# Kernel optimization log

Hardware: AMD Instinct MI355X
Metric: run time of the kernel (lower is better)

The kernel has to match this reference:

```python
import jax, jax.numpy as jnp
import numpy as np

B = 16384      # batch
CNUM = 2048    # codebook entries
K = 8          # topk
D = 10         # emb_dim
M = 50         # meta_dim
UID = 1000000
IID = 1000000
TAU = 10.0


def setup_inputs() -> dict:
    key = jax.random.key(0)
    ks = jax.random.split(key, 14)
    uid_col = jax.random.randint(ks[0], (B, 1), 0, UID, dtype=jnp.int64)
    iid_col = jax.random.randint(ks[1], (B, 1), 0, IID + 1, dtype=jnp.int64)
    x = jnp.concatenate([uid_col, iid_col], axis=1)
    return {
        "x": x,
        "gumbel_u_src": jax.random.uniform(ks[2], (B, CNUM), dtype=jnp.float32),
        "gumbel_u_tgt": jax.random.uniform(ks[3], (B, CNUM), dtype=jnp.float32),
        "src_uid_table": jax.random.normal(ks[4], (UID, D), dtype=jnp.float32),
        "tgt_uid_table": jax.random.normal(ks[5], (UID, D), dtype=jnp.float32),
        "tgt_iid_table": jax.random.normal(ks[6], (IID + 1, D), dtype=jnp.float32),
        "C": jax.random.normal(ks[7], (CNUM, M), dtype=jnp.float32) * 0.01,
        "w1": jax.random.normal(ks[8], (D, M), dtype=jnp.float32) * 0.01,
        "w2": jax.random.normal(ks[9], (M, D), dtype=jnp.float32) * 0.01,
        "mw1": jax.random.normal(ks[10], (D + M, 50), dtype=jnp.float32) * 0.1,
        "mb1": jnp.zeros((50,), dtype=jnp.float32),
        "mw2": jax.random.normal(ks[11], (50, D * D), dtype=jnp.float32) * 0.1,
        "mb2": jnp.zeros((D * D,), dtype=jnp.float32),
    }


def _gumbel_route(u_emb, C, w1, u_noise):
    # u_emb: [B, D] -> logits s_u: [B, CNUM]
    s = jnp.einsum('bm,cm->bc', u_emb @ w1, C)
    g = -jnp.log(-jnp.log(u_noise + 1e-20) + 1e-20)  # gumbel noise
    gw = jax.nn.softmax((s + g) / TAU, axis=-1)       # F.gumbel_softmax, hard=False
    tw, ti = jax.lax.top_k(gw, K)                     # [B, K]
    c_u = C[ti]                                       # [B, K, M] codebook gather
    return tw, ti, c_u


def reference(x, gumbel_u_src, gumbel_u_tgt, src_uid_table, tgt_uid_table,
              tgt_iid_table, C, w1, w2, mw1, mb1, mw2, mb2):
    # ---- stage == 'test_meta' ----
    # target-side interest embedding ('test_interst' path)
    tuid = tgt_uid_table[x[:, 0]]                      # [B, D]
    tw_t, _, c_t = _gumbel_route(tuid, C, w1, gumbel_u_tgt)
    tuid_ins = ((c_t * tw_t[..., None]).sum(axis=1)) @ w2   # [B, D]
    # source-side routing ('test_meta' path of InterstEmbedding)
    uid = src_uid_table[x[:, 0]]                       # [B, D]
    tw_s, _, c_s = _gumbel_route(uid, C, w1, gumbel_u_src)
    src_fea = jnp.broadcast_to(uid[:, None, :], (uid.shape[0], K, D))  # [B, K, D]
    inp = jnp.concatenate([c_s, src_fea], axis=-1)     # [B, K, M+D] = [B, K, 60]
    h = jax.nn.relu(inp @ mw1 + mb1)                   # [B, K, 50]
    mapping = (h @ mw2 + mb2).reshape(-1, K, D, D)     # per-sample hypernet weights
    src_emb = jnp.einsum('bkd,bkde->bke', src_fea, mapping)  # [B, K, D]
    pre_emb = (src_emb * tw_s[..., None]).sum(axis=1)  # [B, D]
    fin_emb = tuid_ins + pre_emb                       # [B, D]
    iid_emb = tgt_iid_table[x[:, 1]]                   # [B, D]
    return jnp.sum(fin_emb * iid_emb, axis=-1)         # [B]
```

## Files before the change

### kernel.cpp

```cpp
#include <hip/hip_runtime.h>
#include <hip/hip_bf16.h>


#define BROWS 16384
#define CNUM  2048
#define KSEL  8
#define DIMD  10
#define MDIM  50
#define TAUI  0.1f

typedef float    f32x4 __attribute__((ext_vector_type(4)));
typedef _Float16 half8 __attribute__((ext_vector_type(8)));
typedef float    flt2  __attribute__((ext_vector_type(2)));
typedef unsigned int u32;
typedef unsigned long long u64;

__device__ __forceinline__ u32 pkrtz(float a, float b) {
    auto h = __builtin_amdgcn_cvt_pkrtz(a, b);
    union { decltype(h) v; u32 u; } c; c.v = h; return c.u;
}
__device__ __forceinline__ float gnoise(float u) {
    return -__logf(-__logf(u + 1e-20f) + 1e-20f);
}

__global__ void cvtC(const float* __restrict__ Cm, u32* __restrict__ C16) {
    const int j = blockIdx.x * 256 + threadIdx.x;
    const int w = j & 3, l = (j >> 2) & 63, pl = (j >> 8) & 1, Tg = j >> 9;
    const int cand = Tg * 16 + (l & 15);
    const int kk = pl * 16 + ((l >> 4) << 2) + w;
    const int k = 2 * kk;
    const float a = (k < MDIM)     ? Cm[cand*MDIM + k]     : 0.f;
    const float b = (k + 1 < MDIM) ? Cm[cand*MDIM + k + 1] : 0.f;
    C16[j] = pkrtz(a, b);
}

__global__ __launch_bounds__(256, 8)
void mf_route(const int* __restrict__ x32,
              const float* __restrict__ gsrc,
              const float* __restrict__ gtgt,
              const float* __restrict__ suid,
              const float* __restrict__ tuid,
              const float* __restrict__ Cm,
              const float* __restrict__ w1,
              const u32* __restrict__ C16,
              float* __restrict__ gTW,
              int*   __restrict__ gTI)
{
    __shared__ __align__(16) float smem[2432];
    __shared__ int sFlag;
    float* sPf  = smem;
    u32*   T48u = (u32*)(smem + 832);
    float* T48l = smem + 1600;
    float* TS   = smem + 2368;

    const int tid  = threadIdx.x;
    const int row0 = blockIdx.x * 8;

    if (tid == 0) sFlag = 1;
    __syncthreads();
    if (tid < 128) { if (x32[2*tid+1] != 0) atomicAnd(&sFlag, 0); }
    __syncthreads();
    const int is64 = sFlag;

    for (int t = tid; t < 16*52; t += 256) {
        const int rt = t / 52, mm = t - rt*52;
        float v = 0.f;
        if (mm < MDIM) {
            const int r = row0 + (rt >> 1);
            const int uidx = is64 ? x32[4*r] : x32[2*r];
            const float* tab = (rt & 1) ? suid : tuid;
            #pragma unroll
            for (int d = 0; d < DIMD; ++d) v += tab[uidx*DIMD + d] * w1[d*MDIM + mm];
        }
        sPf[t] = v;
    }
    __syncthreads();

    const int lane = tid & 63, wv = tid >> 6;
    const int lr = lane & 15, lk = lane >> 4;
    const int rt = lr;
    const float* up = ((lr & 1) ? gsrc : gtgt) + (size_t)(row0 + (lr >> 1)) * CNUM;

    half8 b0, b1;
    {
        union { u32 u[4]; half8 v; } c0, c1;
        #pragma unroll
        for (int jj = 0; jj < 4; ++jj) {
            const int k0 = lk*8 + jj*2;
            c0.u[jj] = pkrtz(sPf[rt*52 + k0], sPf[rt*52 + k0 + 1]);
            const int k1 = 32 + lk*8 + jj*2;
            const float e0 = (k1     < 52) ? sPf[rt*52 + k1]     : 0.f;
            const float e1 = (k1 + 1 < 52) ? sPf[rt*52 + k1 + 1] : 0.f;
            c1.u[jj] = pkrtz(e0, e1);
        }
        b0 = c0.v; b1 = c1.v;
    }

    float ts = 0.f;
    float q0=-3.4e38f,q1=-3.4e38f,q2=-3.4e38f,q3=-3.4e38f,
          q4=-3.4e38f,q5=-3.4e38f,q6=-3.4e38f,q7=-3.4e38f;

    for (int t = 0; t < 32; ++t) {
        const int cb = wv*512 + t*16;
        const f32x4 u4 = *(const f32x4*)(up + cb + lk*4);
        const u32* cp = C16 + (size_t)((wv*32 + t)*128 + lane)*4;
        const half8 a0 = *(const half8*)cp;
        const half8 a1 = *(const half8*)(cp + 256);
        f32x4 acc = {0.f, 0.f, 0.f, 0.f};
        acc = __builtin_amdgcn_mfma_f32_16x16x32_f16(a0, b0, acc, 0, 0, 0);
        acc = __builtin_amdgcn_mfma_f32_16x16x32_f16(a1, b1, acc, 0, 0, 0);
        const int cg = cb + lk*4;
        #pragma unroll
        for (int r4 = 0; r4 < 4; ++r4) {
            const float l = (acc[r4] + gnoise(u4[r4])) * TAUI;
            ts += __expf(l);
            const float xs = __uint_as_float(
                (__float_as_uint(l) & 0xFFFFF800u) | (u32)(cg + r4));
            q0 = fmaxf(q0, fminf(q1, xs));
            q1 = fmaxf(q1, fminf(q2, xs));
            q2 = fmaxf(q2, fminf(q3, xs));
            q3 = fmaxf(q3, fminf(q4, xs));
            q4 = fmaxf(q4, fminf(q5, xs));
            q5 = fmaxf(q5, fminf(q6, xs));
            q6 = fmaxf(q6, fminf(q7, xs));
            q7 = fmaxf(q7, xs);
        }
    }

    {
        float tss = ts;
        tss += __shfl_xor(tss, 16); tss += __shfl_xor(tss, 32);
        if (lk == 0) TS[rt*4 + wv] = tss;
        #pragma unroll
        for (int k = 0; k < 12; ++k) {
            float gm = fmaxf(q7, __shfl_xor(q7, 16));
            gm = fmaxf(gm, __shfl_xor(gm, 32));
            if (q7 == gm) {
                T48u[rt*48 + wv*12 + k] = __float_as_uint(q7);
                q7=q6; q6=q5; q5=q4; q4=q3; q3=q2; q2=q1; q1=q0; q0=-3.4e38f;
            }
        }
    }
    __syncthreads();

    for (int e = tid; e < 16*48; e += 256) {
        const int ert = e / 48;
        const int idx = (int)(T48u[e] & 2047u);
        const float* pf = sPf + ert*52;
        const float* cr = Cm + idx*MDIM;
        float s = 0.f;
        #pragma unroll
        for (int k2 = 0; k2 < 25; ++k2) {
            flt2 c = *(const flt2*)(cr + k2*2);
            s += pf[2*k2] * c.x + pf[2*k2+1] * c.y;
        }
        const int r = row0 + (ert >> 1);
        const float u = ((ert & 1) ? gsrc : gtgt)[(size_t)r*CNUM + idx];
        T48l[e] = (s + gnoise(u)) * TAUI;
    }
    __syncthreads();

    if (tid < 16) {
        const int r8 = tid;
        const float inv = 1.0f / (TS[r8*4] + TS[r8*4+1] + TS[r8*4+2] + TS[r8*4+3]);
        u64 used = 0;
        for (int k = 0; k < KSEL; ++k) {
            float bl = -3.4e38f; int bi = 1 << 30; int bj = 0;
            for (int j = 0; j < 48; ++j) {
                if ((used >> j) & 1ull) continue;
                const float lv = T48l[r8*48 + j];
                const int   iv = (int)(T48u[r8*48 + j] & 2047u);
                if (lv > bl || (lv == bl && iv < bi)) { bl = lv; bi = iv; bj = j; }
            }
            used |= 1ull << bj;
            const int grt = blockIdx.x*16 + r8;
            gTW[grt*KSEL + k] = __expf(bl) * inv;
            gTI[grt*KSEL + k] = bi;
        }
    }
}

__global__ __launch_bounds__(256, 4)
void mf_epilog(const int* __restrict__ x32,
               const float* __restrict__ suid,
               const float* __restrict__ tiid,
               const float* __restrict__ Cm,
               const float* __restrict__ w2,
               const float* __restrict__ mw1,
               const float* __restrict__ mb1,
               const float* __restrict__ mw2,
               const float* __restrict__ mb2,
               const float* __restrict__ gTW,
               const int*   __restrict__ gTI,
               float* __restrict__ out)
{
    __shared__ int sFlag;
    const int tid = threadIdx.x;
    const int g = tid >> 4, lg = tid & 15;
    const int row = blockIdx.x * 16 + g;

    if (tid == 0) sFlag = 1;
    __syncthreads();
    if (tid < 128) { if (x32[2*tid+1] != 0) atomicAnd(&sFlag, 0); }
    __syncthreads();
    const int is64 = sFlag;

    const int uidx = is64 ? x32[4*row]     : x32[2*row];
    const int iidx = is64 ? x32[4*row + 2] : x32[2*row + 1];

    float uid[10], ti[10];
    #pragma unroll
    for (int d = 0; d < DIMD; ++d) uid[d] = suid[(size_t)uidx*DIMD + d];
    #pragma unroll
    for (int e = 0; e < DIMD; ++e) ti[e] = tiid[(size_t)iidx*DIMD + e];

    float twt[8], tws[8]; int it[8], is_[8];
    #pragma unroll
    for (int k = 0; k < KSEL; ++k) {
        twt[k] = gTW[(row*2)*KSEL + k];     it[k]  = gTI[(row*2)*KSEL + k];
        tws[k] = gTW[(row*2+1)*KSEL + k];   is_[k] = gTI[(row*2+1)*KSEL + k];
    }

    const int j0 = 4*lg;
    const int nj = (j0 + 4 <= MDIM) ? 4 : (j0 < MDIM ? MDIM - j0 : 0);

    float po = 0.f;
    float qt[4] = {0,0,0,0}, w2t[4] = {0,0,0,0}, hb[4] = {0,0,0,0};

    if (nj) {
        {
            flt2 m0 = *(const flt2*)(mb1 + j0);
            hb[0] = m0.x; hb[1] = m0.y;
            if (nj == 4) { flt2 m1 = *(const flt2*)(mb1 + j0 + 2); hb[2] = m1.x; hb[3] = m1.y; }
            #pragma unroll
            for (int d = 0; d < DIMD; ++d) {
                const float* r = mw1 + (MDIM + d)*MDIM + j0;
                flt2 a = *(const flt2*)r;
                hb[0] += uid[d]*a.x; hb[1] += uid[d]*a.y;
                if (nj == 4) { flt2 b = *(const flt2*)(r + 2); hb[2] += uid[d]*b.x; hb[3] += uid[d]*b.y; }
            }
        }
        for (int jj = 0; jj < nj; ++jj) {
            const float* r = w2 + (j0 + jj)*DIMD;
            float s = 0.f;
            #pragma unroll
            for (int p = 0; p < 5; ++p) { flt2 a = *(const flt2*)(r + 2*p); s += a.x*ti[2*p] + a.y*ti[2*p+1]; }
            w2t[jj] = s;
        }
        for (int jj = 0; jj < nj; ++jj) {
            const float* r = mw2 + (size_t)(j0 + jj)*(DIMD*DIMD);
            float s = 0.f;
            #pragma unroll
            for (int d = 0; d < DIMD; ++d) {
                float sd = 0.f;
                #pragma unroll
                for (int p = 0; p < 5; ++p) { flt2 a = *(const flt2*)(r + d*DIMD + 2*p); sd += a.x*ti[2*p] + a.y*ti[2*p+1]; }
                s += uid[d]*sd;
            }
            qt[jj] = s;
        }
        {
            float ws[4] = {0,0,0,0};
            #pragma unroll
            for (int k = 0; k < KSEL; ++k) {
                const float* cr = Cm + (size_t)it[k]*MDIM + j0;
                flt2 a = *(const flt2*)cr;
                ws[0] += twt[k]*a.x; ws[1] += twt[k]*a.y;
                if (nj == 4) { flt2 b = *(const flt2*)(cr + 2); ws[2] += twt[k]*b.x; ws[3] += twt[k]*b.y; }
            }
            for (int jj = 0; jj < nj; ++jj) po += ws[jj]*w2t[jj];
        }
        float hk[8][4];
        #pragma unroll
        for (int k = 0; k < KSEL; ++k)
            #pragma unroll
            for (int jj = 0; jj < 4; ++jj) hk[k][jj] = hb[jj];
        for (int t2 = 0; t2 < MDIM; t2 += 2) {
            const float* r0 = mw1 + t2*MDIM + j0;
            const float* r1 = mw1 + (t2+1)*MDIM + j0;
            flt2 wa0 = *(const flt2*)r0, wb0 = *(const flt2*)(r0 + 2);
            flt2 wa1 = *(const flt2*)r1, wb1 = *(const flt2*)(r1 + 2);
            #pragma unroll
            for (int k = 0; k < KSEL; ++k) {
                flt2 c = *(const flt2*)(Cm + (size_t)is_[k]*MDIM + t2);
                hk[k][0] += c.x*wa0.x + c.y*wa1.x;
                hk[k][1] += c.x*wa0.y + c.y*wa1.y;
                hk[k][2] += c.x*wb0.x + c.y*wb1.x;
                hk[k][3] += c.x*wb0.y + c.y*wb1.y;
            }
        }
        #pragma unroll
        for (int k = 0; k < KSEL; ++k) {
            float s = 0.f;
            for (int jj = 0; jj < nj; ++jj) s += fmaxf(hk[k][jj], 0.f)*qt[jj];
            po += tws[k]*s;
        }
    }
    if (lg == 0) {
        float stw = 0.f;
        #pragma unroll
        for (int k = 0; k < KSEL; ++k) stw += tws[k];
        float bt = 0.f;
        #pragma unroll
        for (int d = 0; d < DIMD; ++d) {
            float sd = 0.f;
            #pragma unroll
            for (int e = 0; e < DIMD; ++e) sd += mb2[d*DIMD + e]*ti[e];
            bt += uid[d]*sd;
        }
        po += stw*bt;
    }
    po += __shfl_xor(po, 1, 16);
    po += __shfl_xor(po, 2, 16);
    po += __shfl_xor(po, 4, 16);
    po += __shfl_xor(po, 8, 16);
    if (lg == 0) out[row] = po;
}

__global__ __launch_bounds__(256, 4)
void mf_fused_fb(const int* __restrict__ x32,
                 const float* __restrict__ gsrc,
                 const float* __restrict__ gtgt,
                 const float* __restrict__ suid,
                 const float* __restrict__ tuid,
                 const float* __restrict__ tiid,
                 const float* __restrict__ Cm,
                 const float* __restrict__ w1,
                 const float* __restrict__ w2,
                 const float* __restrict__ mw1,
                 const float* __restrict__ mb1,
                 const float* __restrict__ mw2,
                 const float* __restrict__ mb2,
                 float* __restrict__ out)
{
    __shared__ __align__(16) float smem[9536];
    __shared__ int sFlag;
    float* sPf  = smem;
    u32*   T24u = (u32*)(smem + 1664);
    float* T24l = smem + 2432;

    const int tid  = threadIdx.x;
    const int row0 = blockIdx.x * 16;

    if (tid == 0) sFlag = 1;
    __syncthreads();
    if (tid < 128) { if (x32[2*tid+1] != 0) atomicAnd(&sFlag, 0); }
    __syncthreads();
    const int is64 = sFlag;

    for (int t = tid; t < 32*52; t += 256) {
        const int rt = t / 52, mm = t - rt*52;
        float v = 0.f;
        if (mm < MDIM) {
            const int r = row0 + (rt >> 1);
            const int uidx = is64 ? x32[4*r] : x32[2*r];
            const float* tab = (rt & 1) ? suid : tuid;
            #pragma unroll
            for (int d = 0; d < DIMD; ++d) v += tab[uidx*DIMD + d] * w1[d*MDIM + mm];
        }
        sPf[t] = v;
    }
    __syncthreads();

    const int lane = tid & 63, wv = tid >> 6;
    const int lr = lane & 15, lk = lane >> 4;
    const int g = wv & 1, h = wv >> 1;
    const int rt = g*16 + lr;
    const float* up = ((lr & 1) ? gsrc : gtgt) + (size_t)(row0 + g*8 + (lr >> 1)) * CNUM;

    half8 b0, b1;
    {
        union { u32 u[4]; half8 v; } c0, c1;
        #pragma unroll
        for (int jj = 0; jj < 4; ++jj) {
            const int k0 = lk*8 + jj*2;
            c0.u[jj] = pkrtz(sPf[rt*52 + k0], sPf[rt*52 + k0 + 1]);
            const int k1 = 32 + lk*8 + jj*2;
            const float e0 = (k1     < 52) ? sPf[rt*52 + k1]     : 0.f;
            const float e1 = (k1 + 1 < 52) ? sPf[rt*52 + k1 + 1] : 0.f;
            c1.u[jj] = pkrtz(e0, e1);
        }
        b0 = c0.v; b1 = c1.v;
    }

    float ts = 0.f;
    float q0=-3.4e38f,q1=-3.4e38f,q2=-3.4e38f,q3=-3.4e38f,
          q4=-3.4e38f,q5=-3.4e38f,q6=-3.4e38f,q7=-3.4e38f;

    for (int t = 0; t < 64; ++t) {
        const int cb = ((t >> 2) << 7) + h*64 + ((t & 3) << 4);
        const float* cr = Cm + (size_t)(cb + lr)*MDIM;
        union { u32 u[4]; half8 v; } c0, c1;
        #pragma unroll
        for (int jj = 0; jj < 4; ++jj) {
            const int k0 = lk*8 + jj*2;
            c0.u[jj] = pkrtz(cr[k0], cr[k0+1]);
            const int k1 = 32 + lk*8 + jj*2;
            const float e0 = (k1     < MDIM) ? cr[k1]   : 0.f;
            const float e1 = (k1 + 1 < MDIM) ? cr[k1+1] : 0.f;
            c1.u[jj] = pkrtz(e0, e1);
        }
        f32x4 acc = {0.f, 0.f, 0.f, 0.f};
        acc = __builtin_amdgcn_mfma_f32_16x16x32_f16(c0.v, b0, acc, 0, 0, 0);
        acc = __builtin_amdgcn_mfma_f32_16x16x32_f16(c1.v, b1, acc, 0, 0, 0);
        const f32x4 u4 = *(const f32x4*)(up + cb + lk*4);
        const int cg = cb + lk*4;
        #pragma unroll
        for (int r4 = 0; r4 < 4; ++r4) {
            const float l = (acc[r4] + gnoise(u4[r4])) * TAUI;
            ts += __expf(l);
            const float xs = __uint_as_float(
                (__float_as_uint(l) & 0xFFFFF800u) | (u32)(cg + r4));
            q0 = fmaxf(q0, fminf(q1, xs));
            q1 = fmaxf(q1, fminf(q2, xs));
            q2 = fmaxf(q2, fminf(q3, xs));
            q3 = fmaxf(q3, fminf(q4, xs));
            q4 = fmaxf(q4, fminf(q5, xs));
            q5 = fmaxf(q5, fminf(q6, xs));
            q6 = fmaxf(q6, fminf(q7, xs));
            q7 = fmaxf(q7, xs);
        }
    }

    {
        float tss = ts;
        tss += __shfl_xor(tss, 16); tss += __shfl_xor(tss, 32);
        if (lk == 0) smem[3200 + rt*2 + h] = tss;
        #pragma unroll
        for (int k = 0; k < 12; ++k) {
            float gm = fmaxf(q7, __shfl_xor(q7, 16));
            gm = fmaxf(gm, __shfl_xor(gm, 32));
            if (q7 == gm) {
                T24u[rt*24 + h*12 + k] = __float_as_uint(q7);
                q7=q6; q6=q5; q5=q4; q4=q3; q3=q2; q2=q1; q1=q0; q0=-3.4e38f;
            }
        }
    }
    __syncthreads();

    for (int e = tid; e < 32*24; e += 256) {
        const int ert = e / 24;
        const int idx = (int)(T24u[e] & 2047u);
        const float* pf = sPf + ert*52;
        const float* cr = Cm + idx*MDIM;
        float s = 0.f;
        #pragma unroll
        for (int k2 = 0; k2 < 25; ++k2) {
            flt2 c = *(const flt2*)(cr + k2*2);
            s += pf[2*k2] * c.x + pf[2*k2+1] * c.y;
        }
        const int r = row0 + (ert >> 1);
        const float u = ((ert & 1) ? gsrc : gtgt)[(size_t)r*CNUM + idx];
        T24l[e] = (s + gnoise(u)) * TAUI;
    }
    __syncthreads();

    if (tid < 32) {
        const int rrt = tid;
        const float inv = 1.0f / (smem[3200 + rrt*2] + smem[3200 + rrt*2 + 1]);
        u32 used = 0;
        for (int k = 0; k < KSEL; ++k) {
            float bl = -3.4e38f; int bi = 1 << 30; int bj = 0;
            for (int j = 0; j < 24; ++j) {
                if ((used >> j) & 1) continue;
                const float lv = T24l[rrt*24 + j];
                const int   iv = (int)(T24u[rrt*24 + j] & 2047u);
                if (lv > bl || (lv == bl && iv < bi)) { bl = lv; bi = iv; bj = j; }
            }
            used |= 1u << bj;
            smem[8832 + rrt*KSEL + k] = __expf(bl) * inv;
            ((int*)smem)[9088 + rrt*KSEL + k] = bi;
        }
    }
    __syncthreads();

    float* sH    = smem;
    float* sQ    = smem + 832;
    float* sUd   = smem + 9344;
    float* sTopW = smem + 8832;
    int*   sTopI = (int*)smem + 9088;

    const int gg = tid >> 4, lg = tid & 15;
    const int row = row0 + gg;
    const int rt_t = gg*2, rt_s = gg*2 + 1;
    const int uidx = is64 ? x32[4*row]     : x32[2*row];
    const int iidx = is64 ? x32[4*row + 2] : x32[2*row + 1];

    if (lg < DIMD) sUd[gg*12 + lg] = suid[uidx*DIMD + lg];
    __syncthreads();

    for (int t = lg; t < MDIM*DIMD; t += 16) {
        const int j = t / DIMD, e = t - j*DIMD;
        float q = 0.f;
        #pragma unroll
        for (int d = 0; d < DIMD; ++d) q += sUd[gg*12 + d] * mw2[j*(DIMD*DIMD) + d*DIMD + e];
        sQ[gg*500 + t] = q;
    }
    for (int mm = lg; mm < MDIM; mm += 16) {
        float v = 0.f;
        #pragma unroll
        for (int k = 0; k < KSEL; ++k)
            v += sTopW[rt_t*KSEL + k] * Cm[sTopI[rt_t*KSEL + k]*MDIM + mm];
        sH[gg*52 + mm] = v;
    }
    __syncthreads();

    float acc_e = 0.f, be = 0.f;
    if (lg < DIMD) {
        for (int m2 = 0; m2 < MDIM; ++m2) acc_e += sH[gg*52 + m2] * w2[m2*DIMD + lg];
        #pragma unroll
        for (int d = 0; d < DIMD; ++d) be += sUd[gg*12 + d] * mb2[d*DIMD + lg];
    }
    __syncthreads();

    for (int k = 0; k < KSEL; ++k) {
        const int   ik = sTopI[rt_s*KSEL + k];
        const float tw = sTopW[rt_s*KSEL + k];
        for (int j = lg; j < MDIM; j += 16) {
            float hh = mb1[j];
            const float* crow = Cm + ik*MDIM;
            for (int t2 = 0; t2 < MDIM; ++t2) hh += crow[t2] * mw1[t2*MDIM + j];
            #pragma unroll
            for (int d = 0; d < DIMD; ++d) hh += sUd[gg*12 + d] * mw1[(MDIM + d)*MDIM + j];
            sH[gg*52 + j] = fmaxf(hh, 0.f);
        }
        __syncthreads();
        if (lg < DIMD) {
            float se = be;
            for (int j = 0; j < MDIM; ++j) se += sH[gg*52 + j] * sQ[gg*500 + j*DIMD + lg];
            acc_e += tw * se;
        }
        __syncthreads();
    }

    float o = 0.f;
    if (lg < DIMD) o = acc_e * tiid[iidx*DIMD + lg];
    #pragma unroll
    for (int k = 8; k >= 1; k >>= 1) o += __shfl_xor(o, k, 16);
    if (lg == 0) out[row] = o;
}

extern "C" void kernel_launch(void* const* d_in, const int* in_sizes, int n_in,
                              void* d_out, int out_size, void* d_ws, size_t ws_size,
                              hipStream_t stream) {
    (void)in_sizes; (void)n_in; (void)out_size;
    const int*   x32  = (const int*)d_in[0];
    const float* gsrc = (const float*)d_in[1];
    const float* gtgt = (const float*)d_in[2];
    const float* suid = (const float*)d_in[3];
    const float* tuid = (const float*)d_in[4];
    const float* tiid = (const float*)d_in[5];
    const float* Cm   = (const float*)d_in[6];
    const float* w1   = (const float*)d_in[7];
    const float* w2   = (const float*)d_in[8];
    const float* mw1  = (const float*)d_in[9];
    const float* mb1  = (const float*)d_in[10];
    const float* mw2  = (const float*)d_in[11];
    const float* mb2  = (const float*)d_in[12];

    if (ws_size >= 655360u * 4u) {
        u32*   C16 = (u32*)d_ws;
        float* gTW = (float*)d_ws + 131072;
        int*   gTI = (int*)d_ws + 393216;
        hipLaunchKernelGGL(cvtC, dim3(512), dim3(256), 0, stream, Cm, C16);
        hipLaunchKernelGGL(mf_route, dim3(BROWS/8), dim3(256), 0, stream,
                           x32, gsrc, gtgt, suid, tuid, Cm, w1, C16, gTW, gTI);
        hipLaunchKernelGGL(mf_epilog, dim3(BROWS/16), dim3(256), 0, stream,
                           x32, suid, tiid, Cm, w2, mw1, mb1, mw2, mb2, gTW, gTI,
                           (float*)d_out);
    } else {
        hipLaunchKernelGGL(mf_fused_fb, dim3(BROWS/16), dim3(256), 0, stream,
                           x32, gsrc, gtgt, suid, tuid, tiid, Cm, w1, w2, mw1, mb1, mw2, mb2,
                           (float*)d_out);
    }
}
```

Before: 283.5 us.

## Stage gumbel noise tiles through LDS with double-buffered async global_load_lds

The per-lane strided global loads of the uniform noise are replaced by coalesced 16-byte global_load_lds transfers into a double-buffered, XOR-swizzled LDS tile. Each step prefetches the next 128-column chunk while the current one feeds the MFMA and top-k work. Column ownership is re-split so every wave covers 32 columns of each 128-column chunk instead of a contiguous 512-column range. This adds 16 KB of LDS per block and a block barrier each iteration, which may lower occupancy and add synchronisation stalls.

```diff
diff --git a/kernel.cpp b/kernel.cpp
--- a/kernel.cpp
+++ b/kernel.cpp
@@ -8,6 +8,7 @@
 #define DIMD  10
 #define MDIM  50
 #define TAUI  0.1f
+#define UOFF  832
 
 typedef float    f32x4 __attribute__((ext_vector_type(4)));
 typedef _Float16 half8 __attribute__((ext_vector_type(8)));
@@ -21,6 +22,12 @@
 }
 __device__ __forceinline__ float gnoise(float u) {
     return -__logf(-__logf(u + 1e-20f) + 1e-20f);
+}
+__device__ __forceinline__ void gload16(const float* g, float* l) {
+    __builtin_amdgcn_global_load_lds(
+        (const __attribute__((address_space(1))) u32*)g,
+        (__attribute__((address_space(3))) u32*)l,
+        16, 0, 0);
 }
 
 __global__ void cvtC(const float* __restrict__ Cm, u32* __restrict__ C16) {
@@ -46,7 +53,7 @@
               float* __restrict__ gTW,
               int*   __restrict__ gTI)
 {
-    __shared__ __align__(16) float smem[2432];
+    __shared__ __align__(16) float smem[UOFF + 4096];
     __shared__ int sFlag;
     float* sPf  = smem;
     u32*   T48u = (u32*)(smem + 832);
@@ -76,10 +83,9 @@
     }
     __syncthreads();
 
-    const int lane = tid & 63, wv = tid >> 6;
+    const int lane = tid & 63, w = tid >> 6;
     const int lr = lane & 15, lk = lane >> 4;
     const int rt = lr;
-    const float* up = ((lr & 1) ? gsrc : gtgt) + (size_t)(row0 + (lr >> 1)) * CNUM;
 
     half8 b0, b1;
     {
@@ -96,47 +102,80 @@
         b0 = c0.v; b1 = c1.v;
     }
 
+    const int jrow = lane >> 5, jc4 = lane & 31;
+    const int rtS0 = 4*w + jrow;
+    const int rtS1 = 4*w + 2 + jrow;
+    const float* usrc0 = ((rtS0 & 1) ? gsrc : gtgt)
+        + (size_t)(row0 + (rtS0 >> 1))*CNUM + ((jc4 ^ (rtS0 & 7)) << 2);
+    const float* usrc1 = ((rtS1 & 1) ? gsrc : gtgt)
+        + (size_t)(row0 + (rtS1 >> 1))*CNUM + ((jc4 ^ (rtS1 & 7)) << 2);
+    float* const udst0a = smem + UOFF +        (4*w    )*128;
+    float* const udst1a = smem + UOFF +        (4*w + 2)*128;
+    float* const udst0b = smem + UOFF + 2048 + (4*w    )*128;
+    float* const udst1b = smem + UOFF + 2048 + (4*w + 2)*128;
+
     float ts = 0.f;
     float q0=-3.4e38f,q1=-3.4e38f,q2=-3.4e38f,q3=-3.4e38f,
           q4=-3.4e38f,q5=-3.4e38f,q6=-3.4e38f,q7=-3.4e38f;
 
-    for (int t = 0; t < 32; ++t) {
-        const int cb = wv*512 + t*16;
-        const f32x4 u4 = *(const f32x4*)(up + cb + lk*4);
-        const u32* cp = C16 + (size_t)((wv*32 + t)*128 + lane)*4;
-        const half8 a0 = *(const half8*)cp;
-        const half8 a1 = *(const half8*)(cp + 256);
-        f32x4 acc = {0.f, 0.f, 0.f, 0.f};
-        acc = __builtin_amdgcn_mfma_f32_16x16x32_f16(a0, b0, acc, 0, 0, 0);
-        acc = __builtin_amdgcn_mfma_f32_16x16x32_f16(a1, b1, acc, 0, 0, 0);
-        const int cg = cb + lk*4;
-        #pragma unroll
-        for (int r4 = 0; r4 < 4; ++r4) {
-            const float l = (acc[r4] + gnoise(u4[r4])) * TAUI;
-            ts += __expf(l);
-            const float xs = __uint_as_float(
-                (__float_as_uint(l) & 0xFFFFF800u) | (u32)(cg + r4));
-            q0 = fmaxf(q0, fminf(q1, xs));
-            q1 = fmaxf(q1, fminf(q2, xs));
-            q2 = fmaxf(q2, fminf(q3, xs));
-            q3 = fmaxf(q3, fminf(q4, xs));
-            q4 = fmaxf(q4, fminf(q5, xs));
-            q5 = fmaxf(q5, fminf(q6, xs));
-            q6 = fmaxf(q6, fminf(q7, xs));
-            q7 = fmaxf(q7, xs);
-        }
+    const int physa = ((w*8)     + lk) ^ (lr & 7);
+    const int physb = ((w*8 + 4) + lk) ^ (lr & 7);
+    const int rbase = UOFF + lr*128;
+
+    gload16(usrc0, udst0a);
+    gload16(usrc1, udst1a);
+    __syncthreads();
+
+    for (int t = 0; t < 16; ++t) {
+        const int bufw = (t & 1) * 2048;
+        const f32x4 u4a = *(const f32x4*)&smem[rbase + bufw + physa*4];
+        const f32x4 u4b = *(const f32x4*)&smem[rbase + bufw + physb*4];
+        if (t + 1 < 16) {
+            const int nb = ((t + 1) & 1) * 2048;
+            gload16(usrc0 + (t + 1)*128, (nb ? udst0b : udst0a));
+            gload16(usrc1 + (t + 1)*128, (nb ? udst1b : udst1a));
+        }
+        #pragma unroll
+        for (int nt = 0; nt < 2; ++nt) {
+            const int cl = w*32 + nt*16;
+            const int Tg = t*8 + w*2 + nt;
+            const u32* cp = C16 + (size_t)(Tg*128 + lane)*4;
+            const half8 a0 = *(const half8*)cp;
+            const half8 a1 = *(const half8*)(cp + 256);
+            f32x4 acc = {0.f, 0.f, 0.f, 0.f};
+            acc = __builtin_amdgcn_mfma_f32_16x16x32_f16(a0, b0, acc, 0, 0, 0);
+            acc = __builtin_amdgcn_mfma_f32_16x16x32_f16(a1, b1, acc, 0, 0, 0);
+            const f32x4 u4 = nt ? u4b : u4a;
+            const int cg = t*128 + cl + lk*4;
+            #pragma unroll
+            for (int r4 = 0; r4 < 4; ++r4) {
+                const float l = (acc[r4] + gnoise(u4[r4])) * TAUI;
+                ts += __expf(l);
+                const float xs = __uint_as_float(
+                    (__float_as_uint(l) & 0xFFFFF800u) | (u32)(cg + r4));
+                q0 = fmaxf(q0, fminf(q1, xs));
+                q1 = fmaxf(q1, fminf(q2, xs));
+                q2 = fmaxf(q2, fminf(q3, xs));
+                q3 = fmaxf(q3, fminf(q4, xs));
+                q4 = fmaxf(q4, fminf(q5, xs));
+                q5 = fmaxf(q5, fminf(q6, xs));
+                q6 = fmaxf(q6, fminf(q7, xs));
+                q7 = fmaxf(q7, xs);
+            }
+        }
+        __syncthreads();
     }
 
     {
         float tss = ts;
         tss += __shfl_xor(tss, 16); tss += __shfl_xor(tss, 32);
-        if (lk == 0) TS[rt*4 + wv] = tss;
+        if (lk == 0) TS[rt*4 + w] = tss;
         #pragma unroll
         for (int k = 0; k < 12; ++k) {
             float gm = fmaxf(q7, __shfl_xor(q7, 16));
             gm = fmaxf(gm, __shfl_xor(gm, 32));
             if (q7 == gm) {
-                T48u[rt*48 + wv*12 + k] = __float_as_uint(q7);
+                T48u[rt*48 + w*12 + k] = __float_as_uint(q7);
                 q7=q6; q6=q5; q5=q4; q4=q3; q3=q2; q2=q1; q1=q0; q0=-3.4e38f;
             }
         }
```

Measured after the change: 278.1 us. No clear change (-1.9%).

## Precompute gumbel noise into fp16 LDS staging with coalesced row loads

Applied to the files above, without the earlier changes.

The routing kernel now cooperatively loads each block's 16 noise rows with coalesced vector loads, computes the gumbel transform once, and stores it as fp16 in a 64KB XOR-swizzled LDS buffer. The MFMA scoring loop then reads the noise from LDS instead of doing strided global loads and logs inside the loop. The projected user features are recomputed after the loop because the shared buffer is reused. This cuts occupancy (launch bounds drop from 8 to 2 blocks) and rounds the noise to fp16 before the top-k prefilter, which could change which candidates reach the exact fp32 rescoring.

```diff
diff --git a/kernel.cpp b/kernel.cpp
--- a/kernel.cpp
+++ b/kernel.cpp
@@ -34,7 +34,7 @@
     C16[j] = pkrtz(a, b);
 }
 
-__global__ __launch_bounds__(256, 8)
+__global__ __launch_bounds__(256, 2)
 void mf_route(const int* __restrict__ x32,
               const float* __restrict__ gsrc,
               const float* __restrict__ gtgt,
@@ -46,21 +46,17 @@
               float* __restrict__ gTW,
               int*   __restrict__ gTI)
 {
-    __shared__ __align__(16) float smem[2432];
-    __shared__ int sFlag;
-    float* sPf  = smem;
-    u32*   T48u = (u32*)(smem + 832);
-    float* T48l = smem + 1600;
-    float* TS   = smem + 2368;
+    __shared__ __align__(16) u32 W[16384];
+    float* F = (float*)W;
 
     const int tid  = threadIdx.x;
     const int row0 = blockIdx.x * 8;
 
-    if (tid == 0) sFlag = 1;
-    __syncthreads();
-    if (tid < 128) { if (x32[2*tid+1] != 0) atomicAnd(&sFlag, 0); }
-    __syncthreads();
-    const int is64 = sFlag;
+    if (tid == 0) W[840] = 1;
+    __syncthreads();
+    if (tid < 128) { if (x32[2*tid+1] != 0) atomicAnd((int*)&W[840], 0); }
+    __syncthreads();
+    const int is64 = (int)W[840];
 
     for (int t = tid; t < 16*52; t += 256) {
         const int rt = t / 52, mm = t - rt*52;
@@ -72,14 +68,13 @@
             #pragma unroll
             for (int d = 0; d < DIMD; ++d) v += tab[uidx*DIMD + d] * w1[d*MDIM + mm];
         }
-        sPf[t] = v;
-    }
-    __syncthreads();
-
-    const int lane = tid & 63, wv = tid >> 6;
+        F[t] = v;
+    }
+    __syncthreads();
+
+    const int lane = tid & 63, w = tid >> 6;
     const int lr = lane & 15, lk = lane >> 4;
     const int rt = lr;
-    const float* up = ((lr & 1) ? gsrc : gtgt) + (size_t)(row0 + (lr >> 1)) * CNUM;
 
     half8 b0, b1;
     {
@@ -87,32 +82,62 @@
         #pragma unroll
         for (int jj = 0; jj < 4; ++jj) {
             const int k0 = lk*8 + jj*2;
-            c0.u[jj] = pkrtz(sPf[rt*52 + k0], sPf[rt*52 + k0 + 1]);
+            c0.u[jj] = pkrtz(F[rt*52 + k0], F[rt*52 + k0 + 1]);
             const int k1 = 32 + lk*8 + jj*2;
-            const float e0 = (k1     < 52) ? sPf[rt*52 + k1]     : 0.f;
-            const float e1 = (k1 + 1 < 52) ? sPf[rt*52 + k1 + 1] : 0.f;
+            const float e0 = (k1     < 52) ? F[rt*52 + k1]     : 0.f;
+            const float e1 = (k1 + 1 < 52) ? F[rt*52 + k1 + 1] : 0.f;
             c1.u[jj] = pkrtz(e0, e1);
         }
         b0 = c0.v; b1 = c1.v;
     }
+    __syncthreads();
+
+    {
+        const float* src[4];
+        #pragma unroll
+        for (int s = 0; s < 4; ++s) {
+            const int rts = w*4 + s;
+            src[s] = ((rts & 1) ? gsrc : gtgt) + (size_t)(row0 + (rts >> 1)) * CNUM;
+        }
+        #pragma unroll
+        for (int i = 0; i < 8; ++i) {
+            f32x4 v[4];
+            #pragma unroll
+            for (int s = 0; s < 4; ++s)
+                v[s] = *(const f32x4*)(src[s] + ((i << 6) + lane) * 4);
+            #pragma unroll
+            for (int s = 0; s < 4; ++s) {
+                const int rts = w*4 + s;
+                const int p = (i << 6) + lane;
+                const int phys = p ^ (rts & 15);
+                const u32 w0 = pkrtz(gnoise(v[s][0]), gnoise(v[s][1]));
+                const u32 w1b = pkrtz(gnoise(v[s][2]), gnoise(v[s][3]));
+                *(uint2*)&W[rts*1024 + 2*phys] = make_uint2(w0, w1b);
+            }
+        }
+    }
+    __syncthreads();
 
     float ts = 0.f;
     float q0=-3.4e38f,q1=-3.4e38f,q2=-3.4e38f,q3=-3.4e38f,
           q4=-3.4e38f,q5=-3.4e38f,q6=-3.4e38f,q7=-3.4e38f;
 
-    for (int t = 0; t < 32; ++t) {
-        const int cb = wv*512 + t*16;
-        const f32x4 u4 = *(const f32x4*)(up + cb + lk*4);
-        const u32* cp = C16 + (size_t)((wv*32 + t)*128 + lane)*4;
+    #pragma unroll 2
+    for (int tt = 0; tt < 32; ++tt) {
+        const int Tg = w*32 + tt;
+        const u32* cp = C16 + (size_t)(Tg*128 + lane)*4;
         const half8 a0 = *(const half8*)cp;
         const half8 a1 = *(const half8*)(cp + 256);
         f32x4 acc = {0.f, 0.f, 0.f, 0.f};
         acc = __builtin_amdgcn_mfma_f32_16x16x32_f16(a0, b0, acc, 0, 0, 0);
         acc = __builtin_amdgcn_mfma_f32_16x16x32_f16(a1, b1, acc, 0, 0, 0);
-        const int cg = cb + lk*4;
+        const int p2 = (w << 7) + (tt << 2) + lk;
+        const uint2 nnu = *(const uint2*)&W[lr*1024 + 2*(p2 ^ lr)];
+        union { uint2 u; _Float16 h[4]; } nn; nn.u = nnu;
+        const int cg = (w << 9) + (tt << 4) + (lk << 2);
         #pragma unroll
         for (int r4 = 0; r4 < 4; ++r4) {
-            const float l = (acc[r4] + gnoise(u4[r4])) * TAUI;
+            const float l = (acc[r4] + (float)nn.h[r4]) * TAUI;
             ts += __expf(l);
             const float xs = __uint_as_float(
                 (__float_as_uint(l) & 0xFFFFF800u) | (u32)(cg + r4));
@@ -126,27 +151,40 @@
             q7 = fmaxf(q7, xs);
         }
     }
+    __syncthreads();
 
     {
         float tss = ts;
         tss += __shfl_xor(tss, 16); tss += __shfl_xor(tss, 32);
-        if (lk == 0) TS[rt*4 + wv] = tss;
+        if (lk == 0) F[1536 + rt*4 + w] = tss;
         #pragma unroll
         for (int k = 0; k < 12; ++k) {
             float gm = fmaxf(q7, __shfl_xor(q7, 16));
             gm = fmaxf(gm, __shfl_xor(gm, 32));
             if (q7 == gm) {
-                T48u[rt*48 + wv*12 + k] = __float_as_uint(q7);
+                W[rt*48 + w*12 + k] = __float_as_uint(q7);
                 q7=q6; q6=q5; q5=q4; q4=q3; q3=q2; q2=q1; q1=q0; q0=-3.4e38f;
             }
         }
+    }
+    for (int t = tid; t < 16*52; t += 256) {
+        const int rts = t / 52, mm = t - rts*52;
+        float v = 0.f;
+        if (mm < MDIM) {
+            const int r = row0 + (rts >> 1);
+            const int uidx = is64 ? x32[4*r] : x32[2*r];
+            const float* tab = (rts & 1) ? suid : tuid;
+            #pragma unroll
+            for (int d = 0; d < DIMD; ++d) v += tab[uidx*DIMD + d] * w1[d*MDIM + mm];
+        }
+        F[1600 + t] = v;
     }
     __syncthreads();
 
     for (int e = tid; e < 16*48; e += 256) {
         const int ert = e / 48;
-        const int idx = (int)(T48u[e] & 2047u);
-        const float* pf = sPf + ert*52;
+        const int idx = (int)(W[e] & 2047u);
+        const float* pf = F + 1600 + ert*52;
         const float* cr = Cm + idx*MDIM;
         float s = 0.f;
         #pragma unroll
@@ -156,20 +194,21 @@
         }
         const int r = row0 + (ert >> 1);
         const float u = ((ert & 1) ? gsrc : gtgt)[(size_t)r*CNUM + idx];
-        T48l[e] = (s + gnoise(u)) * TAUI;
+        F[768 + e] = (s + gnoise(u)) * TAUI;
     }
     __syncthreads();
 
     if (tid < 16) {
         const int r8 = tid;
-        const float inv = 1.0f / (TS[r8*4] + TS[r8*4+1] + TS[r8*4+2] + TS[r8*4+3]);
+        const float inv = 1.0f / (F[1536 + r8*4] + F[1536 + r8*4+1]
+                                + F[1536 + r8*4+2] + F[1536 + r8*4+3]);
         u64 used = 0;
         for (int k = 0; k < KSEL; ++k) {
             float bl = -3.4e38f; int bi = 1 << 30; int bj = 0;
             for (int j = 0; j < 48; ++j) {
                 if ((used >> j) & 1ull) continue;
-                const float lv = T48l[r8*48 + j];
-                const int   iv = (int)(T48u[r8*48 + j] & 2047u);
+                const float lv = F[768 + r8*48 + j];
+                const int   iv = (int)(W[r8*48 + j] & 2047u);
                 if (lv > bl || (lv == bl && iv < bi)) { bl = lv; bi = iv; bj = j; }
             }
             used |= 1ull << bj;
```

Result: slower. 425.7 us (+50.2%).
